# Kernel optimization log

Measured on AMD Instinct MI355X. Metric: run time of the kernel, lower is better.

## Reference

```python
import jax, jax.numpy as jnp
import numpy as np

B, V, H_DIM, W_DIM = 4, 4, 256, 384
D_SH = 1  # sh_degree=0, pred_color=False -> (0+1)^2
SCALE_MIN, SCALE_MAX = 1e-05, 30.0
EPS = 1e-08


def _quat_to_mat(q):  # (...,4) wxyz unit quat -> (...,3,3)
    w, x, y, z = q[..., 0], q[..., 1], q[..., 2], q[..., 3]
    return jnp.stack([
        jnp.stack([1 - 2 * (y * y + z * z), 2 * (x * y - w * z), 2 * (x * z + w * y)], -1),
        jnp.stack([2 * (x * y + w * z), 1 - 2 * (x * x + z * z), 2 * (y * z - w * x)], -1),
        jnp.stack([2 * (x * z - w * y), 2 * (y * z + w * x), 1 - 2 * (x * x + y * y)], -1),
    ], -2)


def _mat_to_quat_wxyz(m):  # (...,3,3) rotation -> (...,4) wxyz
    m00, m01, m02 = m[..., 0, 0], m[..., 0, 1], m[..., 0, 2]
    m10, m11, m12 = m[..., 1, 0], m[..., 1, 1], m[..., 1, 2]
    m20, m21, m22 = m[..., 2, 0], m[..., 2, 1], m[..., 2, 2]
    q_abs = jnp.sqrt(jnp.maximum(0.0, jnp.stack([
        1.0 + m00 + m11 + m22, 1.0 + m00 - m11 - m22,
        1.0 - m00 + m11 - m22, 1.0 - m00 - m11 + m22], -1)))
    cand = jnp.stack([
        jnp.stack([q_abs[..., 0] ** 2, m21 - m12, m02 - m20, m10 - m01], -1),
        jnp.stack([m21 - m12, q_abs[..., 1] ** 2, m10 + m01, m02 + m20], -1),
        jnp.stack([m02 - m20, m10 + m01, q_abs[..., 2] ** 2, m12 + m21], -1),
        jnp.stack([m10 - m01, m20 + m02, m21 + m12, q_abs[..., 3] ** 2], -1),
    ], -2)
    cand = cand / (2.0 * jnp.maximum(q_abs[..., None], 0.1))
    idx = jnp.argmax(q_abs, axis=-1)
    q = jnp.take_along_axis(cand, idx[..., None, None], axis=-2)[..., 0, :]
    return q / jnp.linalg.norm(q, axis=-1, keepdims=True)


def _quat_mul_wxyz(a, b):
    aw, ax, ay, az = a[..., 0], a[..., 1], a[..., 2], a[..., 3]
    bw, bx, by, bz = b[..., 0], b[..., 1], b[..., 2], b[..., 3]
    return jnp.stack([
        aw * bw - ax * bx - ay * by - az * bz,
        aw * bx + ax * bw + ay * bz - az * by,
        aw * by - ax * bz + ay * bw + az * bx,
        aw * bz + ax * by - ay * bx + az * bw], -1)


def setup_inputs() -> dict:
    key = jax.random.key(0)
    k1, k2, k3, k4, k5, k6 = jax.random.split(key, 6)
    # valid world->cam extrinsics: rotation from random unit quats + translation
    q = jax.random.normal(k1, (B, V, 4), jnp.float32)
    q = q / jnp.linalg.norm(q, axis=-1, keepdims=True)
    R = _quat_to_mat(q)
    t = jax.random.normal(k2, (B, V, 3), jnp.float32)
    ext = jnp.zeros((B, V, 4, 4), jnp.float32)
    ext = ext.at[..., :3, :3].set(R).at[..., :3, 3].set(t).at[..., 3, 3].set(1.0)
    # pixel-unit intrinsics
    f = W_DIM * (0.8 + 0.4 * jax.random.uniform(k3, (B, V), jnp.float32))
    intr = jnp.zeros((B, V, 3, 3), jnp.float32)
    intr = (intr.at[..., 0, 0].set(f).at[..., 1, 1].set(f)
                .at[..., 0, 2].set(W_DIM / 2).at[..., 1, 2].set(H_DIM / 2)
                .at[..., 2, 2].set(1.0))
    depths = 0.5 + 9.5 * jax.random.uniform(k4, (B, V, H_DIM, W_DIM), jnp.float32)
    opac = jax.random.uniform(k5, (B, V, H_DIM, W_DIM), jnp.float32)
    raw = jax.random.normal(k6, (B, V, H_DIM, W_DIM, 12), jnp.float32)
    return {"extrinsics": ext, "intrinsics": intr, "depths": depths,
            "opacities": opac, "raw_gaussians": raw, "H": H_DIM, "W": W_DIM}


def reference(extrinsics, intrinsics, depths, opacities, raw_gaussians, H, W):
    raw = raw_gaussians
    b, v = raw.shape[:2]
    dtype = raw.dtype
    # cam2world = affine inverse of world2cam extrinsics
    Rw2c = extrinsics[..., :3, :3]
    t = extrinsics[..., :3, 3]
    Rc2w = jnp.swapaxes(Rw2c, -1, -2)                       # (b,v,3,3)
    origins = -jnp.einsum('bvij,bvj->bvi', Rc2w, t)          # (b,v,3) camera centers
    # normalized intrinsics (detached in the original)
    intr_n = jax.lax.stop_gradient(intrinsics) * jnp.array(
        [[1.0 / W], [1.0 / H], [1.0]], dtype=intrinsics.dtype)
    # pixel-center grid in normalized [0,1] coords, (x, y) order
    xs = (jnp.arange(W, dtype=dtype) + 0.5) / W
    ys = (jnp.arange(H, dtype=dtype) + 0.5) / H
    xy = jnp.stack(jnp.meshgrid(xs, ys, indexing='xy'), -1)  # (H,W,2)
    pixel_size = jnp.array([1.0 / W, 1.0 / H], dtype=dtype)
    xy = xy[None, None] + raw[..., :2] * pixel_size          # (b,v,H,W,2) with xy offset
    # unproject: K^-1 @ [x,y,1], normalize, rotate into world
    Kinv = jnp.linalg.inv(intr_n)                            # (b,v,3,3)
    homog = jnp.concatenate([xy, jnp.ones_like(xy[..., :1])], -1)
    d_cam = jnp.einsum('bvij,bvhwj->bvhwi', Kinv, homog)
    d_cam = d_cam / jnp.linalg.norm(d_cam, axis=-1, keepdims=True)
    d_world = jnp.einsum('bvij,bvhwj->bvhwi', Rc2w, d_cam)
    means = origins[:, :, None, None] + d_world * depths[..., None]
    means = means.reshape(b, -1, 3)
    # scales: sigmoid squash then metric scaling by depth * intrinsics multiplier
    scales = SCALE_MIN + (SCALE_MAX - SCALE_MIN) * jax.nn.sigmoid(raw[..., 2:5])
    k2 = intr_n[..., :2, :2]
    det = k2[..., 0, 0] * k2[..., 1, 1] - k2[..., 0, 1] * k2[..., 1, 0]
    inv2 = jnp.stack([
        jnp.stack([k2[..., 1, 1], -k2[..., 0, 1]], -1),
        jnp.stack([-k2[..., 1, 0], k2[..., 0, 0]], -1)], -2) / det[..., None, None]
    mult = 0.1 * jnp.einsum('bvij,j->bvi', inv2, pixel_size).sum(-1)  # (b,v)
    gs_scales = (scales * depths[..., None] * mult[:, :, None, None, None]).reshape(b, -1, 3)
    # rotations: normalize predicted cam quat (xyzw), compose with c2w rotation -> world wxyz
    rot = raw[..., 5:9]
    rot = rot / (jnp.linalg.norm(rot, axis=-1, keepdims=True) + EPS)
    cam_q_wxyz = jnp.concatenate([rot[..., 3:4], rot[..., :3]], -1)
    c2w_q = _mat_to_quat_wxyz(Rc2w)                          # (b,v,4)
    world_q = _quat_mul_wxyz(c2w_q[:, :, None, None, :], cam_q_wxyz)
    rotations = world_q.reshape(b, -1, 4)
    # spherical harmonics: degree 0 -> sh_mask is all ones, no SH rotation
    harmonics = raw[..., 9:12].reshape(b, -1, 3, D_SH)
    opac = opacities.reshape(b, -1)
    return means, gs_scales, rotations, harmonics, opac
```

## Files before the change

### kernel.cpp

```cpp
#include <hip/hip_runtime.h>
#include <math.h>

#define Bc 4
#define Vc 4
#define Hc 256
#define Wc 384
#define HWc (Hc*Wc)
#define TOTc (Bc*Vc*HWc)
#define SCALE_MIN_c 1e-05f
#define SCALE_MAX_c 30.0f
#define EPS_c 1e-08f

#define MEANS_OFF  ((size_t)0)
#define SCALES_OFF ((size_t)TOTc*3)
#define ROT_OFF    ((size_t)TOTc*6)
#define HARM_OFF   ((size_t)TOTc*10)
#define OPAC_OFF   ((size_t)TOTc*13)

__device__ __forceinline__ void async_copy16(const float4* g, float4* l) {
    __builtin_amdgcn_global_load_lds(
        (const __attribute__((address_space(1))) void*)g,
        (__attribute__((address_space(3))) void*)l,
        16, 0, 0);
}

__global__ __launch_bounds__(256, 6) void ga_kernel(
    const float* __restrict__ ext,
    const float* __restrict__ intr,
    const float* __restrict__ depths,
    const float* __restrict__ opac,
    const float* __restrict__ raw,
    float* __restrict__ out)
{
    __shared__ float4 sRaw[768];

    const int tid  = threadIdx.x;
    const int lane = tid & 63;
    const int wv   = tid >> 6;
    const int g    = blockIdx.x * 256 + tid;

    {
        const float4* gbase = reinterpret_cast<const float4*>(raw)
                            + (size_t)blockIdx.x * 768 + wv * 192;
        float4* lbase = &sRaw[wv * 192];
        async_copy16(gbase +   0 + lane, lbase +   0);
        async_copy16(gbase +  64 + lane, lbase +  64);
        async_copy16(gbase + 128 + lane, lbase + 128);
    }

    const float dep = depths[g];
    const float op  = opac[g];

    const int view = blockIdx.x / (HWc / 256);
    const float* E = ext  + view * 16;
    const float* I = intr + view * 9;

    const float R0 = E[0], R1 = E[4], R2 = E[8];
    const float R3 = E[1], R4 = E[5], R5 = E[9];
    const float R6 = E[2], R7 = E[6], R8 = E[10];
    const float t0 = E[3], t1 = E[7], t2 = E[11];
    const float O0 = -(R0*t0 + R1*t1 + R2*t2);
    const float O1 = -(R3*t0 + R4*t1 + R5*t2);
    const float O2 = -(R6*t0 + R7*t1 + R8*t2);

    const float a00 = I[0]*(1.0f/Wc), a01 = I[1]*(1.0f/Wc), a02 = I[2]*(1.0f/Wc);
    const float a10 = I[3]*(1.0f/Hc), a11 = I[4]*(1.0f/Hc), a12 = I[5]*(1.0f/Hc);
    const float a20 = I[6],           a21 = I[7],           a22 = I[8];
    const float det = a00*(a11*a22 - a12*a21)
                    - a01*(a10*a22 - a12*a20)
                    + a02*(a10*a21 - a11*a20);
    const float id = 1.0f / det;
    const float K0 = (a11*a22 - a12*a21)*id;
    const float K1 = (a02*a21 - a01*a22)*id;
    const float K2 = (a01*a12 - a02*a11)*id;
    const float K3 = (a12*a20 - a10*a22)*id;
    const float K4 = (a00*a22 - a02*a20)*id;
    const float K5 = (a02*a10 - a00*a12)*id;
    const float K6 = (a10*a21 - a11*a20)*id;
    const float K7 = (a01*a20 - a00*a21)*id;
    const float K8 = (a00*a11 - a01*a10)*id;

    const float det2 = a00*a11 - a01*a10;
    const float mult = 0.1f * ((a11*(1.0f/Wc) - a01*(1.0f/Hc))
                             + (-a10*(1.0f/Wc) + a00*(1.0f/Hc))) / det2;

    const float m00 = R0, m01 = R1, m02 = R2;
    const float m10 = R3, m11 = R4, m12 = R5;
    const float m20 = R6, m21 = R7, m22 = R8;
    const float qa0 = sqrtf(fmaxf(0.0f, 1.0f + m00 + m11 + m22));
    const float qa1 = sqrtf(fmaxf(0.0f, 1.0f + m00 - m11 - m22));
    const float qa2 = sqrtf(fmaxf(0.0f, 1.0f - m00 + m11 - m22));
    const float qa3 = sqrtf(fmaxf(0.0f, 1.0f - m00 - m11 + m22));
    float bq = qa0;
    float b0 = qa0*qa0, b1 = m21 - m12, b2 = m02 - m20, b3 = m10 - m01;
    {
        const bool s1 = qa1 > bq;
        b0 = s1 ? (m21 - m12) : b0;
        b1 = s1 ? (qa1*qa1)   : b1;
        b2 = s1 ? (m10 + m01) : b2;
        b3 = s1 ? (m02 + m20) : b3;
        bq = s1 ? qa1 : bq;
        const bool s2 = qa2 > bq;
        b0 = s2 ? (m02 - m20) : b0;
        b1 = s2 ? (m10 + m01) : b1;
        b2 = s2 ? (qa2*qa2)   : b2;
        b3 = s2 ? (m12 + m21) : b3;
        bq = s2 ? qa2 : bq;
        const bool s3 = qa3 > bq;
        b0 = s3 ? (m10 - m01) : b0;
        b1 = s3 ? (m20 + m02) : b1;
        b2 = s3 ? (m21 + m12) : b2;
        b3 = s3 ? (qa3*qa3)   : b3;
        bq = s3 ? qa3 : bq;
    }
    const float dd = 1.0f / (2.0f * fmaxf(bq, 0.1f));
    const float q0 = b0*dd, q1 = b1*dd, q2 = b2*dd, q3 = b3*dd;
    const float qn = 1.0f / sqrtf(q0*q0 + q1*q1 + q2*q2 + q3*q3);
    const float aw = q0*qn, ax = q1*qn, ay = q2*qn, az = q3*qn;

    asm volatile("s_waitcnt vmcnt(0)" ::: "memory");

    const float4 r0 = sRaw[tid*3 + 0];
    const float4 r1 = sRaw[tid*3 + 1];
    const float4 r2 = sRaw[tid*3 + 2];

    const int pix = g % HWc;
    const int h = pix / Wc;
    const int w = pix - h * Wc;

    const float x = (w + 0.5f) * (1.0f/Wc) + r0.x * (1.0f/Wc);
    const float y = (h + 0.5f) * (1.0f/Hc) + r0.y * (1.0f/Hc);

    float dc0 = K0*x + K1*y + K2;
    float dc1 = K3*x + K4*y + K5;
    float dc2 = K6*x + K7*y + K8;
    const float inl = rsqrtf(dc0*dc0 + dc1*dc1 + dc2*dc2);
    dc0 *= inl; dc1 *= inl; dc2 *= inl;

    const float dw0 = R0*dc0 + R1*dc1 + R2*dc2;
    const float dw1 = R3*dc0 + R4*dc1 + R5*dc2;
    const float dw2 = R6*dc0 + R7*dc1 + R8*dc2;

    const float sm  = dep * mult;
    const float sc0 = (SCALE_MIN_c + (SCALE_MAX_c - SCALE_MIN_c) / (1.0f + __expf(-r0.z))) * sm;
    const float sc1 = (SCALE_MIN_c + (SCALE_MAX_c - SCALE_MIN_c) / (1.0f + __expf(-r0.w))) * sm;
    const float sc2 = (SCALE_MIN_c + (SCALE_MAX_c - SCALE_MIN_c) / (1.0f + __expf(-r1.x))) * sm;

    const float rx = r1.y, ry = r1.z, rz = r1.w, rw = r2.x;
    const float rn = 1.0f / (sqrtf(rx*rx + ry*ry + rz*rz + rw*rw) + EPS_c);
    const float bwq = rw*rn, bxq = rx*rn, byq = ry*rn, bzq = rz*rn;
    float4 wq;
    wq.x = aw*bwq - ax*bxq - ay*byq - az*bzq;
    wq.y = aw*bxq + ax*bwq + ay*bzq - az*byq;
    wq.z = aw*byq - ax*bzq + ay*bwq + az*bxq;
    wq.w = aw*bzq + ax*byq - ay*bxq + az*bwq;
    reinterpret_cast<float4*>(out + ROT_OFF)[g] = wq;

    out[OPAC_OFF + g] = op;

    float4 A, Bv;
    A.x = O0 + dw0*dep;  A.y = O1 + dw1*dep;  A.z = O2 + dw2*dep;  A.w = sc0;
    Bv.x = sc1;  Bv.y = sc2;  Bv.z = r2.y;  Bv.w = r2.z;
    sRaw[tid*3 + 0] = A;
    sRaw[tid*3 + 1] = Bv;
    reinterpret_cast<float*>(sRaw)[tid*12 + 8] = r2.w;

    const float* sF = reinterpret_cast<const float*>(sRaw);
    float* outM = out + MEANS_OFF  + (size_t)blockIdx.x * 768;
    float* outS = out + SCALES_OFF + (size_t)blockIdx.x * 768;
    float* outH = out + HARM_OFF   + (size_t)blockIdx.x * 768;
    #pragma unroll
    for (int k = 0; k < 3; ++k) {
        const int off  = wv*192 + k*64 + lane;
        const int p    = off / 3;
        const int c    = off - p*3;
        const int base = p*12 + c;
        outM[off] = sF[base + 0];
        outS[off] = sF[base + 3];
        outH[off] = sF[base + 6];
    }
}

extern "C" void kernel_launch(void* const* d_in, const int* in_sizes, int n_in,
                              void* d_out, int out_size, void* d_ws, size_t ws_size,
                              hipStream_t stream) {
    const float* ext    = (const float*)d_in[0];
    const float* intr   = (const float*)d_in[1];
    const float* depths = (const float*)d_in[2];
    const float* opac   = (const float*)d_in[3];
    const float* raw    = (const float*)d_in[4];
    float* out = (float*)d_out;

    ga_kernel<<<TOTc / 256, 256, 0, stream>>>(ext, intr, depths, opac, raw, out);
}
```

Before: 170.6 us.

## Process four pixels per thread with direct float4 loads and stores

Each thread now handles four consecutive pixels, loading its 48 raw floats as twelve float4 vector loads and writing means, scales, harmonics and rotations as packed float4 stores. This removes the LDS staging through global_load_lds and the strided scalar transpose stores, and spreads the per-view setup work over four pixels. The grid shrinks to a quarter of the blocks and the launch bound hint drops to 4. The cost is more registers per thread and less parallelism, and each thread's loads are strided across lanes (48 bytes apart), which may reduce coalescing efficiency.

```diff
diff --git a/kernel.cpp b/kernel.cpp
--- a/kernel.cpp
+++ b/kernel.cpp
@@ -17,14 +17,7 @@
 #define HARM_OFF   ((size_t)TOTc*10)
 #define OPAC_OFF   ((size_t)TOTc*13)
 
-__device__ __forceinline__ void async_copy16(const float4* g, float4* l) {
-    __builtin_amdgcn_global_load_lds(
-        (const __attribute__((address_space(1))) void*)g,
-        (__attribute__((address_space(3))) void*)l,
-        16, 0, 0);
-}
-
-__global__ __launch_bounds__(256, 6) void ga_kernel(
+__global__ __launch_bounds__(256, 4) void ga_kernel(
     const float* __restrict__ ext,
     const float* __restrict__ intr,
     const float* __restrict__ depths,
@@ -32,28 +25,21 @@
     const float* __restrict__ raw,
     float* __restrict__ out)
 {
-    __shared__ float4 sRaw[768];
+    const int tid = threadIdx.x;
+    const int T   = blockIdx.x * 256 + tid;
+    const int bview   = blockIdx.x / 96;
+    const int pixBase = (blockIdx.x - bview * 96) * 1024 + (tid << 2);
 
-    const int tid  = threadIdx.x;
-    const int lane = tid & 63;
-    const int wv   = tid >> 6;
-    const int g    = blockIdx.x * 256 + tid;
+    const float4* rb = reinterpret_cast<const float4*>(raw) + (size_t)T * 12;
+    const float4 v0 = rb[0],  v1 = rb[1],  v2  = rb[2];
+    const float4 v3 = rb[3],  v4 = rb[4],  v5  = rb[5];
+    const float4 v6 = rb[6],  v7 = rb[7],  v8  = rb[8];
+    const float4 v9 = rb[9],  v10 = rb[10], v11 = rb[11];
+    const float4 d4 = reinterpret_cast<const float4*>(depths)[T];
+    const float4 o4 = reinterpret_cast<const float4*>(opac)[T];
 
-    {
-        const float4* gbase = reinterpret_cast<const float4*>(raw)
-                            + (size_t)blockIdx.x * 768 + wv * 192;
-        float4* lbase = &sRaw[wv * 192];
-        async_copy16(gbase +   0 + lane, lbase +   0);
-        async_copy16(gbase +  64 + lane, lbase +  64);
-        async_copy16(gbase + 128 + lane, lbase + 128);
-    }
-
-    const float dep = depths[g];
-    const float op  = opac[g];
-
-    const int view = blockIdx.x / (HWc / 256);
-    const float* E = ext  + view * 16;
-    const float* I = intr + view * 9;
+    const float* E = ext  + bview * 16;
+    const float* I = intr + bview * 9;
 
     const float R0 = E[0], R1 = E[4], R2 = E[8];
     const float R3 = E[1], R4 = E[5], R5 = E[9];
@@ -84,32 +70,29 @@
     const float mult = 0.1f * ((a11*(1.0f/Wc) - a01*(1.0f/Hc))
                              + (-a10*(1.0f/Wc) + a00*(1.0f/Hc))) / det2;
 
-    const float m00 = R0, m01 = R1, m02 = R2;
-    const float m10 = R3, m11 = R4, m12 = R5;
-    const float m20 = R6, m21 = R7, m22 = R8;
-    const float qa0 = sqrtf(fmaxf(0.0f, 1.0f + m00 + m11 + m22));
-    const float qa1 = sqrtf(fmaxf(0.0f, 1.0f + m00 - m11 - m22));
-    const float qa2 = sqrtf(fmaxf(0.0f, 1.0f - m00 + m11 - m22));
-    const float qa3 = sqrtf(fmaxf(0.0f, 1.0f - m00 - m11 + m22));
+    const float qa0 = sqrtf(fmaxf(0.0f, 1.0f + R0 + R4 + R8));
+    const float qa1 = sqrtf(fmaxf(0.0f, 1.0f + R0 - R4 - R8));
+    const float qa2 = sqrtf(fmaxf(0.0f, 1.0f - R0 + R4 - R8));
+    const float qa3 = sqrtf(fmaxf(0.0f, 1.0f - R0 - R4 + R8));
     float bq = qa0;
-    float b0 = qa0*qa0, b1 = m21 - m12, b2 = m02 - m20, b3 = m10 - m01;
+    float b0 = qa0*qa0, b1 = R7 - R5, b2 = R2 - R6, b3 = R3 - R1;
     {
         const bool s1 = qa1 > bq;
-        b0 = s1 ? (m21 - m12) : b0;
+        b0 = s1 ? (R7 - R5)   : b0;
         b1 = s1 ? (qa1*qa1)   : b1;
-        b2 = s1 ? (m10 + m01) : b2;
-        b3 = s1 ? (m02 + m20) : b3;
+        b2 = s1 ? (R3 + R1)   : b2;
+        b3 = s1 ? (R2 + R6)   : b3;
         bq = s1 ? qa1 : bq;
         const bool s2 = qa2 > bq;
-        b0 = s2 ? (m02 - m20) : b0;
-        b1 = s2 ? (m10 + m01) : b1;
+        b0 = s2 ? (R2 - R6)   : b0;
+        b1 = s2 ? (R3 + R1)   : b1;
         b2 = s2 ? (qa2*qa2)   : b2;
-        b3 = s2 ? (m12 + m21) : b3;
+        b3 = s2 ? (R5 + R7)   : b3;
         bq = s2 ? qa2 : bq;
         const bool s3 = qa3 > bq;
-        b0 = s3 ? (m10 - m01) : b0;
-        b1 = s3 ? (m20 + m02) : b1;
-        b2 = s3 ? (m21 + m12) : b2;
+        b0 = s3 ? (R3 - R1)   : b0;
+        b1 = s3 ? (R6 + R2)   : b1;
+        b2 = s3 ? (R7 + R5)   : b2;
         b3 = s3 ? (qa3*qa3)   : b3;
         bq = s3 ? qa3 : bq;
     }
@@ -118,67 +101,70 @@
     const float qn = 1.0f / sqrtf(q0*q0 + q1*q1 + q2*q2 + q3*q3);
     const float aw = q0*qn, ax = q1*qn, ay = q2*qn, az = q3*qn;
 
-    asm volatile("s_waitcnt vmcnt(0)" ::: "memory");
+    reinterpret_cast<float4*>(out + OPAC_OFF)[T] = o4;
 
-    const float4 r0 = sRaw[tid*3 + 0];
-    const float4 r1 = sRaw[tid*3 + 1];
-    const float4 r2 = sRaw[tid*3 + 2];
+    const int   h     = pixBase / Wc;
+    const int   w0    = pixBase - h * Wc;
+    const float ybase = (h + 0.5f) * (1.0f/Hc);
 
-    const int pix = g % HWc;
-    const int h = pix / Wc;
-    const int w = pix - h * Wc;
+    float4* outM = reinterpret_cast<float4*>(out + MEANS_OFF)  + (size_t)T * 3;
+    float4* outS = reinterpret_cast<float4*>(out + SCALES_OFF) + (size_t)T * 3;
+    float4* outH = reinterpret_cast<float4*>(out + HARM_OFF)   + (size_t)T * 3;
+    float4* outR = reinterpret_cast<float4*>(out + ROT_OFF)    + (size_t)T * 4;
 
-    const float x = (w + 0.5f) * (1.0f/Wc) + r0.x * (1.0f/Wc);
-    const float y = (h + 0.5f) * (1.0f/Hc) + r0.y * (1.0f/Hc);
+    auto PIX = [&](const float4 A, const float4 Bq, const float4 C,
+                   const float dep, const int j,
+                   float& mx, float& my, float& mz,
+                   float& s0, float& s1, float& s2) -> float4 {
+        const float x = (w0 + j + 0.5f) * (1.0f/Wc) + A.x * (1.0f/Wc);
+        const float y = ybase + A.y * (1.0f/Hc);
 
-    float dc0 = K0*x + K1*y + K2;
-    float dc1 = K3*x + K4*y + K5;
-    float dc2 = K6*x + K7*y + K8;
-    const float inl = rsqrtf(dc0*dc0 + dc1*dc1 + dc2*dc2);
-    dc0 *= inl; dc1 *= inl; dc2 *= inl;
+        float dc0 = K0*x + K1*y + K2;
+        float dc1 = K3*x + K4*y + K5;
+        float dc2 = K6*x + K7*y + K8;
+        const float inl = rsqrtf(dc0*dc0 + dc1*dc1 + dc2*dc2);
+        dc0 *= inl; dc1 *= inl; dc2 *= inl;
 
-    const float dw0 = R0*dc0 + R1*dc1 + R2*dc2;
-    const float dw1 = R3*dc0 + R4*dc1 + R5*dc2;
-    const float dw2 = R6*dc0 + R7*dc1 + R8*dc2;
+        const float dw0 = R0*dc0 + R1*dc1 + R2*dc2;
+        const float dw1 = R3*dc0 + R4*dc1 + R5*dc2;
+        const float dw2 = R6*dc0 + R7*dc1 + R8*dc2;
 
-    const float sm  = dep * mult;
-    const float sc0 = (SCALE_MIN_c + (SCALE_MAX_c - SCALE_MIN_c) / (1.0f + __expf(-r0.z))) * sm;
-    const float sc1 = (SCALE_MIN_c + (SCALE_MAX_c - SCALE_MIN_c) / (1.0f + __expf(-r0.w))) * sm;
-    const float sc2 = (SCALE_MIN_c + (SCALE_MAX_c - SCALE_MIN_c) / (1.0f + __expf(-r1.x))) * sm;
+        mx = O0 + dw0*dep;  my = O1 + dw1*dep;  mz = O2 + dw2*dep;
 
-    const float rx = r1.y, ry = r1.z, rz = r1.w, rw = r2.x;
-    const float rn = 1.0f / (sqrtf(rx*rx + ry*ry + rz*rz + rw*rw) + EPS_c);
-    const float bwq = rw*rn, bxq = rx*rn, byq = ry*rn, bzq = rz*rn;
-    float4 wq;
-    wq.x = aw*bwq - ax*bxq - ay*byq - az*bzq;
-    wq.y = aw*bxq + ax*bwq + ay*bzq - az*byq;
-    wq.z = aw*byq - ax*bzq + ay*bwq + az*bxq;
-    wq.w = aw*bzq + ax*byq - ay*bxq + az*bwq;
-    reinterpret_cast<float4*>(out + ROT_OFF)[g] = wq;
+        const float sm = dep * mult;
+        s0 = (SCALE_MIN_c + (SCALE_MAX_c - SCALE_MIN_c) / (1.0f + __expf(-A.z))) * sm;
+        s1 = (SCALE_MIN_c + (SCALE_MAX_c - SCALE_MIN_c) / (1.0f + __expf(-A.w))) * sm;
+        s2 = (SCALE_MIN_c + (SCALE_MAX_c - SCALE_MIN_c) / (1.0f + __expf(-Bq.x))) * sm;
 
-    out[OPAC_OFF + g] = op;
+        const float rx = Bq.y, ry = Bq.z, rz = Bq.w, rw = C.x;
+        const float rn = 1.0f / (sqrtf(rx*rx + ry*ry + rz*rz + rw*rw) + EPS_c);
+        const float bwq = rw*rn, bxq = rx*rn, byq = ry*rn, bzq = rz*rn;
+        float4 wq;
+        wq.x = aw*bwq - ax*bxq - ay*byq - az*bzq;
+        wq.y = aw*bxq + ax*bwq + ay*bzq - az*byq;
+        wq.z = aw*byq - ax*bzq + ay*bwq + az*bxq;
+        wq.w = aw*bzq + ax*byq - ay*bxq + az*bwq;
+        return wq;
+    };
 
-    float4 A, Bv;
-    A.x = O0 + dw0*dep;  A.y = O1 + dw1*dep;  A.z = O2 + dw2*dep;  A.w = sc0;
-    Bv.x = sc1;  Bv.y = sc2;  Bv.z = r2.y;  Bv.w = r2.z;
-    sRaw[tid*3 + 0] = A;
-    sRaw[tid*3 + 1] = Bv;
-    reinterpret_cast<float*>(sRaw)[tid*12 + 8] = r2.w;
+    float A0, A1, A2, S0, S1, S2;
+    float C0, C1, C2, E0, E1, E2;
 
-    const float* sF = reinterpret_cast<const float*>(sRaw);
-    float* outM = out + MEANS_OFF  + (size_t)blockIdx.x * 768;
-    float* outS = out + SCALES_OFF + (size_t)blockIdx.x * 768;
-    float* outH = out + HARM_OFF   + (size_t)blockIdx.x * 768;
-    #pragma unroll
-    for (int k = 0; k < 3; ++k) {
-        const int off  = wv*192 + k*64 + lane;
-        const int p    = off / 3;
-        const int c    = off - p*3;
-        const int base = p*12 + c;
-        outM[off] = sF[base + 0];
-        outS[off] = sF[base + 3];
-        outH[off] = sF[base + 6];
-    }
+    outR[0] = PIX(v0, v1, v2,  d4.x, 0, A0, A1, A2, S0, S1, S2);
+    outR[1] = PIX(v3, v4, v5,  d4.y, 1, C0, C1, C2, E0, E1, E2);
+    outM[0] = make_float4(A0, A1, A2, C0);
+    outS[0] = make_float4(S0, S1, S2, E0);
+    outH[0] = make_float4(v2.y, v2.z, v2.w, v5.y);
+
+    outR[2] = PIX(v6, v7, v8,  d4.z, 2, A0, A1, A2, S0, S1, S2);
+    outM[1] = make_float4(C1, C2, A0, A1);
+    outS[1] = make_float4(E1, E2, S0, S1);
+    outH[1] = make_float4(v5.z, v5.w, v8.y, v8.z);
+
+    outR[3] = PIX(v9, v10, v11, d4.w, 3, C0, C1, C2, E0, E1, E2);
+    outM[2] = make_float4(A2, C0, C1, C2);
+    outS[2] = make_float4(S2, E0, E1, E2);
+    outH[2] = make_float4(v8.w, v11.y, v11.z, v11.w);
 }
 
 extern "C" void kernel_launch(void* const* d_in, const int* in_sizes, int n_in,
@@ -191,5 +177,5 @@
     const float* raw    = (const float*)d_in[4];
     float* out = (float*)d_out;
 
-    ga_kernel<<<TOTc / 256, 256, 0, stream>>>(ext, intr, depths, opac, raw, out);
+    ga_kernel<<<TOTc / 1024, 256, 0, stream>>>(ext, intr, depths, opac, raw, out);
 }
```

Result: slower. 221.4 us (+29.8%).
